# Kernel tuning notes

Hardware: AMD Instinct MI355X
Metric: run time of the kernel (lower is better)

The kernel has to match this reference:

```python
import jax, jax.numpy as jnp
import numpy as np

N, D, H, C = 50000, 256, 4, 16  # nodes, in_dim, heads, out_channels (hidden_dim)
E = 1600000
NEG_SLOPE = 0.2


def _gatv2_layer(x, src, dst, Wl, bl, Wr, br, att, bias, n_nodes):
    """PyG GATv2Conv (share_weights=False, concat=True, eval mode).
    x: [N, Fin]; Wl/Wr: [Fin, H*C]; att: [H, C]; bias: [H*C].
    """
    xl = (x @ Wl + bl).reshape(n_nodes, H, C)  # source-side transform
    xr = (x @ Wr + br).reshape(n_nodes, H, C)  # target-side transform
    # per-edge attention logits: a^T LeakyReLU(xl_j + xr_i)
    e = jax.nn.leaky_relu(xl[src] + xr[dst], negative_slope=NEG_SLOPE)  # [E,H,C]
    logits = jnp.einsum('ehc,hc->eh', e, att)  # [E,H]
    # scatter-softmax over incoming edges of each target node
    m = jax.ops.segment_max(logits, dst, num_segments=n_nodes)  # [N,H]
    ex = jnp.exp(logits - m[dst])
    denom = jax.ops.segment_sum(ex, dst, num_segments=n_nodes)  # [N,H]
    alpha = ex / denom[dst]  # [E,H]
    out = jax.ops.segment_sum(alpha[:, :, None] * xl[src], dst, num_segments=n_nodes)
    return out.reshape(n_nodes, H * C) + bias


def setup_inputs() -> dict:
    key = jax.random.key(0)
    ks = jax.random.split(key, 16)
    g = lambda k, shp, fan: jax.random.normal(k, shp, jnp.float32) * (1.0 / np.sqrt(fan))
    inp = {
        'x': jax.random.normal(ks[0], (N, D), jnp.float32),
        'edge_index': jax.random.randint(ks[1], (2, E), 0, N, dtype=jnp.int64),
        # conv1: in D -> H*C
        'Wl1': g(ks[2], (D, H * C), D), 'bl1': jnp.zeros((H * C,), jnp.float32),
        'Wr1': g(ks[3], (D, H * C), D), 'br1': jnp.zeros((H * C,), jnp.float32),
        'att1': g(ks[4], (H, C), C), 'bias1': jnp.zeros((H * C,), jnp.float32),
        # conv2: in H*C -> H*C
        'Wl2': g(ks[5], (H * C, H * C), H * C), 'bl2': jnp.zeros((H * C,), jnp.float32),
        'Wr2': g(ks[6], (H * C, H * C), H * C), 'br2': jnp.zeros((H * C,), jnp.float32),
        'att2': g(ks[7], (H, C), C), 'bias2': jnp.zeros((H * C,), jnp.float32),
        # output head: H*C -> D
        'Wo': g(ks[8], (H * C, D), H * C), 'bo': jnp.zeros((D,), jnp.float32),
    }
    return inp


def reference(x, edge_index, Wl1, bl1, Wr1, br1, att1, bias1,
              Wl2, bl2, Wr2, br2, att2, bias2, Wo, bo):
    src, dst = edge_index[0], edge_index[1]
    h = jax.nn.relu(_gatv2_layer(x, src, dst, Wl1, bl1, Wr1, br1, att1, bias1, N))
    h = jax.nn.relu(_gatv2_layer(h, src, dst, Wl2, bl2, Wr2, br2, att2, bias2, N))
    return jax.nn.sigmoid(h @ Wo + bo)  # min_max is None -> no affine rescale
```

## Files before the change

### kernel.cpp

```cpp
#include <hip/hip_runtime.h>
#include <math.h>

#define NN 50000
#define DIN 256
#define HC 64
#define NEG 0.2f
#define TM 64
#define NB 196
#define EPB 4096
#define CAP 36864

typedef short bf16x8 __attribute__((ext_vector_type(8)));
typedef unsigned short ush8 __attribute__((ext_vector_type(8)));
typedef float f32x4 __attribute__((ext_vector_type(4)));

__device__ __forceinline__ unsigned short f2bf(float x) {
    unsigned u = __float_as_uint(x);
    u += 0x7FFFu + ((u >> 16) & 1u);
    return (unsigned short)(u >> 16);
}
__device__ __forceinline__ float bf2f(unsigned short h) {
    return __uint_as_float((unsigned)h << 16);
}

template <int CTRL>
__device__ __forceinline__ float dpp_mov(float x) {
    int r = __builtin_amdgcn_update_dpp(0, __float_as_int(x), CTRL, 0xF, 0xF, true);
    return __int_as_float(r);
}
__device__ __forceinline__ float reduce16_bcast(float v) {
    v += dpp_mov<0xB1>(v);
    v += dpp_mov<0x4E>(v);
    v += dpp_mov<0x141>(v);
    v += dpp_mov<0x140>(v);
    return v;
}


__global__ __launch_bounds__(256) void bhist_k(const int* __restrict__ dst,
                                               int* __restrict__ bcnt, int E) {
    __shared__ int h[NB];
    int t = threadIdx.x;
    for (int i = t; i < NB; i += 256) h[i] = 0;
    __syncthreads();
    int base = blockIdx.x * 2048 + t;
#pragma unroll
    for (int k = 0; k < 8; ++k) {
        int e = base + k * 256;
        if (e < E) atomicAdd(&h[dst[e] >> 8], 1);
    }
    __syncthreads();
    for (int i = t; i < NB; i += 256)
        if (h[i]) atomicAdd(&bcnt[i], h[i]);
}

__global__ __launch_bounds__(256) void bscan_k(const int* __restrict__ bcnt,
                                               int* __restrict__ boffs,
                                               int* __restrict__ bcursor,
                                               int* __restrict__ offs, int E) {
    __shared__ int s[256];
    int t = threadIdx.x;
    s[t] = (t < NB) ? bcnt[t] : 0;
    __syncthreads();
    for (int off = 1; off < 256; off <<= 1) {
        int v = s[t];
        int u = (t >= off) ? s[t - off] : 0;
        __syncthreads();
        s[t] = v + u;
        __syncthreads();
    }
    if (t < NB) {
        int ex = (t == 0) ? 0 : s[t - 1];
        boffs[t] = ex;
        bcursor[t] = ex;
    }
    if (t == NB) boffs[NB] = s[NB - 1];
    if (t == 0) offs[NN] = E;
}

__global__ __launch_bounds__(1024) void bin_k(const int* __restrict__ src,
                                              const int* __restrict__ dst,
                                              int* __restrict__ bcursor,
                                              unsigned* __restrict__ epair, int E) {
    __shared__ int hist[NB];
    __shared__ int lofs[NB];
    __shared__ int gshift[NB];
    __shared__ int scanb[256];
    __shared__ unsigned pbuf[EPB];
    __shared__ unsigned char abkt[EPB];
    int t = threadIdx.x;
    for (int i = t; i < NB; i += 1024) hist[i] = 0;
    __syncthreads();
    int e0 = blockIdx.x * EPB;
    unsigned p[4]; int bk[4], rk[4]; bool val[4];
#pragma unroll
    for (int k = 0; k < 4; ++k) {
        int e = e0 + k * 1024 + t;
        val[k] = e < E;
        if (val[k]) {
            int s = src[e], d = dst[e];
            p[k] = ((unsigned)s << 8) | (unsigned)(d & 255);
            bk[k] = d >> 8;
            rk[k] = atomicAdd(&hist[bk[k]], 1);
        }
    }
    __syncthreads();
    if (t < 256) scanb[t] = (t < NB) ? hist[t] : 0;
    __syncthreads();
    for (int off = 1; off < 256; off <<= 1) {
        int v = 0, u = 0;
        if (t < 256) { v = scanb[t]; if (t >= off) u = scanb[t - off]; }
        __syncthreads();
        if (t < 256) scanb[t] = v + u;
        __syncthreads();
    }
    if (t < NB) {
        int ex = (t == 0) ? 0 : scanb[t - 1];
        lofs[t] = ex;
        int gb = atomicAdd(&bcursor[t], hist[t]);
        gshift[t] = gb - ex;
    }
    __syncthreads();
    int total = scanb[NB - 1];
#pragma unroll
    for (int k = 0; k < 4; ++k) {
        if (val[k]) {
            int pos = lofs[bk[k]] + rk[k];
            pbuf[pos] = p[k];
            abkt[pos] = (unsigned char)bk[k];
        }
    }
    __syncthreads();
    for (int i = t; i < total; i += 1024) {
        int b = abkt[i];
        epair[gshift[b] + i] = pbuf[i];
    }
}

__global__ __launch_bounds__(1024) void bsort_k(const unsigned* __restrict__ epair,
                                                const int* __restrict__ boffs,
                                                int* __restrict__ offs,
                                                unsigned* __restrict__ ssrc, int n) {
    __shared__ int lhist[256];
    __shared__ int lcur[256];
    __shared__ int scanb[256];
    __shared__ unsigned sbuf[CAP];
    int b = blockIdx.x, t = threadIdx.x;
    int start = boffs[b], end = boffs[b + 1];
    int cnt = end - start;
    if (t < 256) lhist[t] = 0;
    __syncthreads();
    for (int i = t; i < cnt; i += 1024) {
        unsigned p = epair[start + i];
        atomicAdd(&lhist[p & 255], 1);
    }
    __syncthreads();
    if (t < 256) scanb[t] = lhist[t];
    __syncthreads();
    for (int off = 1; off < 256; off <<= 1) {
        int v = 0, u = 0;
        if (t < 256) { v = scanb[t]; if (t >= off) u = scanb[t - off]; }
        __syncthreads();
        if (t < 256) scanb[t] = v + u;
        __syncthreads();
    }
    if (t < 256) {
        int ex = (t == 0) ? 0 : scanb[t - 1];
        lcur[t] = ex;
        int node = b * 256 + t;
        if (node < n) offs[node] = start + ex;
    }
    __syncthreads();
    if (cnt <= CAP) {
        for (int i = t; i < cnt; i += 1024) {
            unsigned p = epair[start + i];
            int r = atomicAdd(&lcur[p & 255], 1);
            sbuf[r] = p & ~255u;
        }
        __syncthreads();
        for (int i = t; i < cnt; i += 1024) ssrc[start + i] = sbuf[i];
    } else {
        for (int i = t; i < cnt; i += 1024) {
            unsigned p = epair[start + i];
            int r = atomicAdd(&lcur[p & 255], 1);
            ssrc[start + r] = p & ~255u;
        }
    }
}

__global__ __launch_bounds__(256) void wprep_dual_k(const float* __restrict__ Wl,
                                                    const float* __restrict__ Wr,
                                                    unsigned short* __restrict__ img,
                                                    int K) {
    int i = blockIdx.x * 256 + threadIdx.x;
    int total = (K >> 5) * 10240;
    if (i >= total) return;
    int kk = i % 40;
    int c  = (i / 40) & 127;
    int p  = (i / 5120) & 1;
    int s  = i / 10240;
    unsigned short v = 0;
    if (kk < 32) {
        int k = s * 32 + kk;
        float w = (c < 64) ? Wl[k * HC + c] : Wr[k * HC + (c - 64)];
        unsigned short hi = f2bf(w);
        v = p ? f2bf(w - bf2f(hi)) : hi;
    }
    img[i] = v;
}

__global__ __launch_bounds__(256) void wprep_head_k(const float* __restrict__ Wo,
                                                    unsigned short* __restrict__ img) {
    int i = blockIdx.x * 256 + threadIdx.x;
    if (i >= 40960) return;
    int kk = i % 40;
    int c  = (i / 40) & 127;
    int p  = (i / 5120) & 1;
    int s  = (i / 10240) & 1;
    int h  = i / 20480;
    unsigned short v = 0;
    if (kk < 32) {
        int k = s * 32 + kk;
        float w = Wo[k * DIN + h * 128 + c];
        unsigned short hi = f2bf(w);
        v = p ? f2bf(w - bf2f(hi)) : hi;
    }
    img[i] = v;
}

__global__ __launch_bounds__(256) void gemm_dual_mfma_k(
        const float* __restrict__ A,
        const unsigned short* __restrict__ img,
        const float* __restrict__ bl, const float* __restrict__ br,
        float* __restrict__ xl, float* __restrict__ xr,
        int n, int K) {
    __shared__ __attribute__((aligned(16))) unsigned short As[2][64][40];
    __shared__ __attribute__((aligned(16))) unsigned short Bs[2][128][40];
    int t = threadIdx.x;
    int l = t & 63, w = t >> 6;
    int wr = w >> 1, wc = w & 1;
    int lan = l & 15;
    int kb  = (l >> 4) * 8;
    int row0 = blockIdx.x * 64;
    int srow = t >> 2;
    int skq  = (t & 3) * 8;
    bool rok = (row0 + srow) < n;
    const float* aptr = A + (size_t)(row0 + srow) * K + skq;

    f32x4 acc0[4] = {}, acc1[4] = {};

    int nks = K >> 5;
    for (int ks = 0; ks < nks; ++ks) {
        __syncthreads();
        {
            const ush8* src = (const ush8*)(img + (size_t)ks * 10240);
            ush8* dst = (ush8*)&Bs[0][0][0];
            int base = w * 5 * 64 + l;
#pragma unroll
            for (int c2 = 0; c2 < 5; ++c2) {
                int u = base + c2 * 64;
                dst[u] = src[u];
            }
        }
        {
            float4 f0 = make_float4(0.f, 0.f, 0.f, 0.f), f1 = f0;
            if (rok) {
                f0 = *(const float4*)(aptr + ks * 32);
                f1 = *(const float4*)(aptr + ks * 32 + 4);
            }
            float xs[8] = {f0.x, f0.y, f0.z, f0.w, f1.x, f1.y, f1.z, f1.w};
            ush8 hi8, lo8;
#pragma unroll
            for (int j = 0; j < 8; ++j) {
                unsigned short h = f2bf(xs[j]);
                hi8[j] = h;
                lo8[j] = f2bf(xs[j] - bf2f(h));
            }
            *(ush8*)&As[0][srow][skq] = hi8;
            *(ush8*)&As[1][srow][skq] = lo8;
        }
        __syncthreads();
        bf16x8 ah0 = *(const bf16x8*)&As[0][wr * 32 + lan][kb];
        bf16x8 ah1 = *(const bf16x8*)&As[0][wr * 32 + 16 + lan][kb];
        bf16x8 al0 = *(const bf16x8*)&As[1][wr * 32 + lan][kb];
        bf16x8 al1 = *(const bf16x8*)&As[1][wr * 32 + 16 + lan][kb];
#pragma unroll
        for (int cf = 0; cf < 4; ++cf) {
            int bc = wc * 64 + cf * 16 + lan;
            bf16x8 bhv = *(const bf16x8*)&Bs[0][bc][kb];
            bf16x8 blv = *(const bf16x8*)&Bs[1][bc][kb];
            acc0[cf] = __builtin_amdgcn_mfma_f32_16x16x32_bf16(ah0, bhv, acc0[cf], 0, 0, 0);
            acc1[cf] = __builtin_amdgcn_mfma_f32_16x16x32_bf16(ah1, bhv, acc1[cf], 0, 0, 0);
            acc0[cf] = __builtin_amdgcn_mfma_f32_16x16x32_bf16(al0, bhv, acc0[cf], 0, 0, 0);
            acc1[cf] = __builtin_amdgcn_mfma_f32_16x16x32_bf16(al1, bhv, acc1[cf], 0, 0, 0);
            acc0[cf] = __builtin_amdgcn_mfma_f32_16x16x32_bf16(ah0, blv, acc0[cf], 0, 0, 0);
            acc1[cf] = __builtin_amdgcn_mfma_f32_16x16x32_bf16(ah1, blv, acc1[cf], 0, 0, 0);
        }
    }
#pragma unroll
    for (int cf = 0; cf < 4; ++cf) {
        int col = wc * 64 + cf * 16 + lan;
        float bv; float* dst; int c2;
        if (col < 64) { bv = bl[col]; dst = xl; c2 = col; }
        else          { bv = br[col - 64]; dst = xr; c2 = col - 64; }
#pragma unroll
        for (int rf = 0; rf < 2; ++rf) {
            f32x4 a = rf ? acc1[cf] : acc0[cf];
            int rbase = row0 + wr * 32 + rf * 16 + (l >> 4) * 4;
#pragma unroll
            for (int r = 0; r < 4; ++r) {
                int grow = rbase + r;
                if (grow < n) dst[(size_t)grow * HC + c2] = a[r] + bv;
            }
        }
    }
}

__global__ __launch_bounds__(256) void head_gemm_mfma_k(
        const float* __restrict__ A,
        const unsigned short* __restrict__ img,
        const float* __restrict__ bo,
        float* __restrict__ out, int n) {
    __shared__ __attribute__((aligned(16))) unsigned short As[2][64][40];
    __shared__ __attribute__((aligned(16))) unsigned short Bs[2][128][40];
    int t = threadIdx.x;
    int l = t & 63, w = t >> 6;
    int wr = w >> 1, wc = w & 1;
    int lan = l & 15;
    int kb  = (l >> 4) * 8;
    int row0 = blockIdx.x * 64;
    int coloff = blockIdx.y * 128;
    const unsigned short* himg = img + (size_t)blockIdx.y * 2 * 10240;
    int srow = t >> 2;
    int skq  = (t & 3) * 8;
    bool rok = (row0 + srow) < n;
    const float* aptr = A + (size_t)(row0 + srow) * HC + skq;

    f32x4 acc0[4] = {}, acc1[4] = {};

    for (int ks = 0; ks < 2; ++ks) {
        __syncthreads();
        {
            const ush8* src = (const ush8*)(himg + (size_t)ks * 10240);
            ush8* dst = (ush8*)&Bs[0][0][0];
            int base = w * 5 * 64 + l;
#pragma unroll
            for (int c2 = 0; c2 < 5; ++c2) {
                int u = base + c2 * 64;
                dst[u] = src[u];
            }
        }
        {
            float4 f0 = make_float4(0.f, 0.f, 0.f, 0.f), f1 = f0;
            if (rok) {
                f0 = *(const float4*)(aptr + ks * 32);
                f1 = *(const float4*)(aptr + ks * 32 + 4);
            }
            float xs[8] = {f0.x, f0.y, f0.z, f0.w, f1.x, f1.y, f1.z, f1.w};
            ush8 hi8, lo8;
#pragma unroll
            for (int j = 0; j < 8; ++j) {
                unsigned short h = f2bf(xs[j]);
                hi8[j] = h;
                lo8[j] = f2bf(xs[j] - bf2f(h));
            }
            *(ush8*)&As[0][srow][skq] = hi8;
            *(ush8*)&As[1][srow][skq] = lo8;
        }
        __syncthreads();
        bf16x8 ah0 = *(const bf16x8*)&As[0][wr * 32 + lan][kb];
        bf16x8 ah1 = *(const bf16x8*)&As[0][wr * 32 + 16 + lan][kb];
        bf16x8 al0 = *(const bf16x8*)&As[1][wr * 32 + lan][kb];
        bf16x8 al1 = *(const bf16x8*)&As[1][wr * 32 + 16 + lan][kb];
#pragma unroll
        for (int cf = 0; cf < 4; ++cf) {
            int bc = wc * 64 + cf * 16 + lan;
            bf16x8 bhv = *(const bf16x8*)&Bs[0][bc][kb];
            bf16x8 blv = *(const bf16x8*)&Bs[1][bc][kb];
            acc0[cf] = __builtin_amdgcn_mfma_f32_16x16x32_bf16(ah0, bhv, acc0[cf], 0, 0, 0);
            acc1[cf] = __builtin_amdgcn_mfma_f32_16x16x32_bf16(ah1, bhv, acc1[cf], 0, 0, 0);
            acc0[cf] = __builtin_amdgcn_mfma_f32_16x16x32_bf16(al0, bhv, acc0[cf], 0, 0, 0);
            acc1[cf] = __builtin_amdgcn_mfma_f32_16x16x32_bf16(al1, bhv, acc1[cf], 0, 0, 0);
            acc0[cf] = __builtin_amdgcn_mfma_f32_16x16x32_bf16(ah0, blv, acc0[cf], 0, 0, 0);
            acc1[cf] = __builtin_amdgcn_mfma_f32_16x16x32_bf16(ah1, blv, acc1[cf], 0, 0, 0);
        }
    }
#pragma unroll
    for (int cf = 0; cf < 4; ++cf) {
        int col = coloff + wc * 64 + cf * 16 + lan;
        float bv = bo[col];
#pragma unroll
        for (int rf = 0; rf < 2; ++rf) {
            f32x4 a = rf ? acc1[cf] : acc0[cf];
            int rbase = row0 + wr * 32 + rf * 16 + (l >> 4) * 4;
#pragma unroll
            for (int r = 0; r < 4; ++r) {
                int grow = rbase + r;
                if (grow < n) {
                    float v = a[r] + bv;
                    out[(size_t)grow * DIN + col] = 1.f / (1.f + __expf(-v));
                }
            }
        }
    }
}

#define EDGE(ii, xx, vv)                                                  \
    {                                                                      \
        unsigned off = ssb[ii] + lane4;                                    \
        xx = *(const float*)(xlb + off);                                   \
        float s = xx + xrv;                                                \
        vv = attv * (s > 0.f ? s : NEG * s);                               \
    }

__global__ __launch_bounds__(256) void agg_k(const float* __restrict__ xl,
                                             const float* __restrict__ xr,
                                             const float* __restrict__ att,
                                             const float* __restrict__ bias,
                                             const int* __restrict__ offs,
                                             const unsigned* __restrict__ ssb,
                                             float* __restrict__ out, int n) {
    int wave = (blockIdx.x * 256 + threadIdx.x) >> 6;
    int lane = threadIdx.x & 63;
    if (wave >= n) return;
    const char* xlb = (const char*)xl;
    unsigned lane4 = (unsigned)lane * 4u;
    float xrv = xr[(size_t)wave * HC + lane];
    float attv = att[lane];
    float acc = 0.f, den = 0.f;
    int lo = __builtin_amdgcn_readfirstlane(offs[wave]);
    int hi = __builtin_amdgcn_readfirstlane(offs[wave + 1]);
    int i = lo;
    for (; i + 8 <= hi; i += 8) {
        float x0, x1, x2, x3, x4, x5, x6, x7;
        float v0, v1, v2, v3, v4, v5, v6, v7;
        EDGE(i + 0, x0, v0); EDGE(i + 1, x1, v1);
        EDGE(i + 2, x2, v2); EDGE(i + 3, x3, v3);
        EDGE(i + 4, x4, v4); EDGE(i + 5, x5, v5);
        EDGE(i + 6, x6, v6); EDGE(i + 7, x7, v7);
        v0 = reduce16_bcast(v0); v1 = reduce16_bcast(v1);
        v2 = reduce16_bcast(v2); v3 = reduce16_bcast(v3);
        v4 = reduce16_bcast(v4); v5 = reduce16_bcast(v5);
        v6 = reduce16_bcast(v6); v7 = reduce16_bcast(v7);
        float e0 = __expf(v0), e1 = __expf(v1), e2 = __expf(v2), e3 = __expf(v3);
        float e4 = __expf(v4), e5 = __expf(v5), e6 = __expf(v6), e7 = __expf(v7);
        den += ((e0 + e1) + (e2 + e3)) + ((e4 + e5) + (e6 + e7));
        acc += e0 * x0; acc += e1 * x1; acc += e2 * x2; acc += e3 * x3;
        acc += e4 * x4; acc += e5 * x5; acc += e6 * x6; acc += e7 * x7;
    }
    for (; i + 4 <= hi; i += 4) {
        float x0, x1, x2, x3, v0, v1, v2, v3;
        EDGE(i + 0, x0, v0); EDGE(i + 1, x1, v1);
        EDGE(i + 2, x2, v2); EDGE(i + 3, x3, v3);
        v0 = reduce16_bcast(v0); v1 = reduce16_bcast(v1);
        v2 = reduce16_bcast(v2); v3 = reduce16_bcast(v3);
        float e0 = __expf(v0), e1 = __expf(v1), e2 = __expf(v2), e3 = __expf(v3);
        den += (e0 + e1) + (e2 + e3);
        acc += e0 * x0; acc += e1 * x1; acc += e2 * x2; acc += e3 * x3;
    }
    for (; i < hi; ++i) {
        float xv, v;
        EDGE(i, xv, v);
        v = reduce16_bcast(v);
        float ex = __expf(v);
        den += ex;
        acc += ex * xv;
    }
    float o = (den > 0.f) ? acc / den : 0.f;
    o += bias[lane];
    out[(size_t)wave * HC + lane] = fmaxf(o, 0.f);
}

extern "C" void kernel_launch(void* const* d_in, const int* in_sizes, int n_in,
                              void* d_out, int out_size, void* d_ws, size_t ws_size,
                              hipStream_t stream) {
    const float* x    = (const float*)d_in[0];
    const int*   ei   = (const int*)d_in[1];
    const float* Wl1  = (const float*)d_in[2];
    const float* bl1  = (const float*)d_in[3];
    const float* Wr1  = (const float*)d_in[4];
    const float* br1  = (const float*)d_in[5];
    const float* att1 = (const float*)d_in[6];
    const float* bias1= (const float*)d_in[7];
    const float* Wl2  = (const float*)d_in[8];
    const float* bl2  = (const float*)d_in[9];
    const float* Wr2  = (const float*)d_in[10];
    const float* br2  = (const float*)d_in[11];
    const float* att2 = (const float*)d_in[12];
    const float* bias2= (const float*)d_in[13];
    const float* Wo   = (const float*)d_in[14];
    const float* bo   = (const float*)d_in[15];
    float* out = (float*)d_out;

    int E = in_sizes[1] / 2;
    const int* srcv = ei;
    const int* dstv = ei + E;

    size_t NF = (size_t)NN * HC;
    float* xl = (float*)d_ws;
    float* xr = xl + NF;
    float* hb = xr + NF;
    int* offs        = (int*)(hb + NF);
    unsigned* ssrc   = (unsigned*)(offs + NN + 1);
    int* boffs   = (int*)(ssrc + E);
    int* bcursor = boffs + NB + 1;
    int* bcnt    = bcursor + NB;
    unsigned* epair = (unsigned*)d_out;
    unsigned short* img1 = (unsigned short*)d_out;
    unsigned short* img2 = img1 + 81920;
    unsigned short* imgh = (unsigned short*)xl;

    hipMemsetAsync(bcnt, 0, NB * sizeof(int), stream);
    bhist_k<<<(E + 2047) / 2048, 256, 0, stream>>>(dstv, bcnt, E);
    bscan_k<<<1, 256, 0, stream>>>(bcnt, boffs, bcursor, offs, E);
    bin_k<<<(E + EPB - 1) / EPB, 1024, 0, stream>>>(srcv, dstv, bcursor, epair, E);
    bsort_k<<<NB, 1024, 0, stream>>>(epair, boffs, offs, ssrc, NN);
    wprep_dual_k<<<320, 256, 0, stream>>>(Wl1, Wr1, img1, DIN);
    wprep_dual_k<<<80, 256, 0, stream>>>(Wl2, Wr2, img2, HC);

    int gb = (NN + TM - 1) / TM;
    gemm_dual_mfma_k<<<gb, 256, 0, stream>>>(x, img1, bl1, br1, xl, xr, NN, DIN);
    agg_k<<<(NN + 3) / 4, 256, 0, stream>>>(xl, xr, att1, bias1, offs, ssrc, hb, NN);
    gemm_dual_mfma_k<<<gb, 256, 0, stream>>>(hb, img2, bl2, br2, xl, xr, NN, HC);
    agg_k<<<(NN + 3) / 4, 256, 0, stream>>>(xl, xr, att2, bias2, offs, ssrc, hb, NN);
    wprep_head_k<<<160, 256, 0, stream>>>(Wo, imgh);
    head_gemm_mfma_k<<<dim3(gb, 2), 256, 0, stream>>>(hb, imgh, bo, out, NN);
}
```

Baseline: 345.4 us.

## Process four edges per wave with float4 lanes in GATv2 aggregation

Restructures the aggregation kernel so each wave splits into four 16-lane quarters, each handling a different edge. Each lane loads a float4 of the source features, which cuts the per-head DPP reduction from four steps to two and lets four edges' gathers be in flight per instruction. Partial sums are combined across quarters with shuffles at the end. Uses exp2 with a log2e-prescaled attention vector, and handles tail edges with masked clamped indices.

```diff
diff --git a/kernel.cpp b/kernel.cpp
--- a/kernel.cpp
+++ b/kernel.cpp
@@ -27,13 +27,6 @@
 __device__ __forceinline__ float dpp_mov(float x) {
     int r = __builtin_amdgcn_update_dpp(0, __float_as_int(x), CTRL, 0xF, 0xF, true);
     return __int_as_float(r);
-}
-__device__ __forceinline__ float reduce16_bcast(float v) {
-    v += dpp_mov<0xB1>(v);
-    v += dpp_mov<0x4E>(v);
-    v += dpp_mov<0x141>(v);
-    v += dpp_mov<0x140>(v);
-    return v;
 }
 
 
@@ -405,12 +398,26 @@
     }
 }
 
-#define EDGE(ii, xx, vv)                                                  \
-    {                                                                      \
-        unsigned off = ssb[ii] + lane4;                                    \
-        xx = *(const float*)(xlb + off);                                   \
-        float s = xx + xrv;                                                \
-        vv = attv * (s > 0.f ? s : NEG * s);                               \
+#define AGRP(EBASE, FULL)                                                     \
+    {                                                                         \
+        int e = (EBASE) + q;                                                  \
+        bool ok = FULL ? true : (e < hi);                                     \
+        int ec = FULL ? e : (ok ? e : (hi - 1));                              \
+        unsigned sb = ssb[ec];                                                \
+        float4 xv = *(const float4*)(xlb + sb + loff);                        \
+        float s0 = xv.x + xrq.x, s1 = xv.y + xrq.y;                           \
+        float s2 = xv.z + xrq.z, s3 = xv.w + xrq.w;                           \
+        float tt = atq.x * fmaxf(s0, NEG * s0);                               \
+        tt = fmaf(atq.y, fmaxf(s1, NEG * s1), tt);                            \
+        tt = fmaf(atq.z, fmaxf(s2, NEG * s2), tt);                            \
+        tt = fmaf(atq.w, fmaxf(s3, NEG * s3), tt);                            \
+        tt += dpp_mov<0xB1>(tt);                                              \
+        tt += dpp_mov<0x4E>(tt);                                              \
+        float ex = exp2f(tt);                                                 \
+        if (!FULL) ex = ok ? ex : 0.f;                                        \
+        den += ex;                                                            \
+        acc.x = fmaf(ex, xv.x, acc.x); acc.y = fmaf(ex, xv.y, acc.y);         \
+        acc.z = fmaf(ex, xv.z, acc.z); acc.w = fmaf(ex, xv.w, acc.w);         \
     }
 
 __global__ __launch_bounds__(256) void agg_k(const float* __restrict__ xl,
@@ -423,52 +430,43 @@
     int wave = (blockIdx.x * 256 + threadIdx.x) >> 6;
     int lane = threadIdx.x & 63;
     if (wave >= n) return;
+    int q  = lane >> 4;
+    int sl = lane & 15;
     const char* xlb = (const char*)xl;
-    unsigned lane4 = (unsigned)lane * 4u;
-    float xrv = xr[(size_t)wave * HC + lane];
-    float attv = att[lane];
-    float acc = 0.f, den = 0.f;
+    unsigned loff = (unsigned)sl * 16u;
+    float4 xrq = *(const float4*)(xr + (size_t)wave * HC + sl * 4);
+    float4 atq = *(const float4*)(att + sl * 4);
+    const float LOG2E = 1.44269504088896340736f;
+    atq.x *= LOG2E; atq.y *= LOG2E; atq.z *= LOG2E; atq.w *= LOG2E;
+    float4 acc = make_float4(0.f, 0.f, 0.f, 0.f);
+    float den = 0.f;
     int lo = __builtin_amdgcn_readfirstlane(offs[wave]);
     int hi = __builtin_amdgcn_readfirstlane(offs[wave + 1]);
     int i = lo;
-    for (; i + 8 <= hi; i += 8) {
-        float x0, x1, x2, x3, x4, x5, x6, x7;
-        float v0, v1, v2, v3, v4, v5, v6, v7;
-        EDGE(i + 0, x0, v0); EDGE(i + 1, x1, v1);
-        EDGE(i + 2, x2, v2); EDGE(i + 3, x3, v3);
-        EDGE(i + 4, x4, v4); EDGE(i + 5, x5, v5);
-        EDGE(i + 6, x6, v6); EDGE(i + 7, x7, v7);
-        v0 = reduce16_bcast(v0); v1 = reduce16_bcast(v1);
-        v2 = reduce16_bcast(v2); v3 = reduce16_bcast(v3);
-        v4 = reduce16_bcast(v4); v5 = reduce16_bcast(v5);
-        v6 = reduce16_bcast(v6); v7 = reduce16_bcast(v7);
-        float e0 = __expf(v0), e1 = __expf(v1), e2 = __expf(v2), e3 = __expf(v3);
-        float e4 = __expf(v4), e5 = __expf(v5), e6 = __expf(v6), e7 = __expf(v7);
-        den += ((e0 + e1) + (e2 + e3)) + ((e4 + e5) + (e6 + e7));
-        acc += e0 * x0; acc += e1 * x1; acc += e2 * x2; acc += e3 * x3;
-        acc += e4 * x4; acc += e5 * x5; acc += e6 * x6; acc += e7 * x7;
-    }
-    for (; i + 4 <= hi; i += 4) {
-        float x0, x1, x2, x3, v0, v1, v2, v3;
-        EDGE(i + 0, x0, v0); EDGE(i + 1, x1, v1);
-        EDGE(i + 2, x2, v2); EDGE(i + 3, x3, v3);
-        v0 = reduce16_bcast(v0); v1 = reduce16_bcast(v1);
-        v2 = reduce16_bcast(v2); v3 = reduce16_bcast(v3);
-        float e0 = __expf(v0), e1 = __expf(v1), e2 = __expf(v2), e3 = __expf(v3);
-        den += (e0 + e1) + (e2 + e3);
-        acc += e0 * x0; acc += e1 * x1; acc += e2 * x2; acc += e3 * x3;
-    }
-    for (; i < hi; ++i) {
-        float xv, v;
-        EDGE(i, xv, v);
-        v = reduce16_bcast(v);
-        float ex = __expf(v);
-        den += ex;
-        acc += ex * xv;
-    }
-    float o = (den > 0.f) ? acc / den : 0.f;
-    o += bias[lane];
-    out[(size_t)wave * HC + lane] = fmaxf(o, 0.f);
+    for (; i + 16 <= hi; i += 16) {
+        AGRP(i, true) AGRP(i + 4, true) AGRP(i + 8, true) AGRP(i + 12, true)
+    }
+    for (; i < hi; i += 4) {
+        AGRP(i, false)
+    }
+#pragma unroll
+    for (int m = 16; m < 64; m <<= 1) {
+        acc.x += __shfl_xor(acc.x, m);
+        acc.y += __shfl_xor(acc.y, m);
+        acc.z += __shfl_xor(acc.z, m);
+        acc.w += __shfl_xor(acc.w, m);
+        den   += __shfl_xor(den, m);
+    }
+    if (q == 0) {
+        float r = (den > 0.f) ? 1.f / den : 0.f;
+        float4 b4 = *(const float4*)(bias + sl * 4);
+        float4 o;
+        o.x = fmaxf(fmaf(acc.x, r, b4.x), 0.f);
+        o.y = fmaxf(fmaf(acc.y, r, b4.y), 0.f);
+        o.z = fmaxf(fmaf(acc.z, r, b4.z), 0.f);
+        o.w = fmaxf(fmaf(acc.w, r, b4.w), 0.f);
+        *(float4*)(out + (size_t)wave * HC + sl * 4) = o;
+    }
 }
 
 extern "C" void kernel_launch(void* const* d_in, const int* in_sizes, int n_in,
```

Result: no change. 350.6 us (+1.5%).
